# Kernel optimization log

Measured on AMD Instinct MI355X. Metric: run time of the kernel, lower is better.

The kernel has to match this reference:

```python
import jax, jax.numpy as jnp
import numpy as np

NUM_STAB = 1e-3  # numerical_stabilizer for relu kernel


def _relu_feature(x, proj):
    # x: [B, L, H, D], proj: [M, D] -> [B, L, H, M]
    ratio = 1.0 / jnp.sqrt(jnp.asarray(proj.shape[0], x.dtype))
    return jax.nn.relu(ratio * jnp.einsum('blhd,md->blhm', x, proj)) + NUM_STAB


def setup_inputs() -> dict:
    key = jax.random.key(0)
    k1, k2, k3, k4, k5 = jax.random.split(key, 5)
    B, L, H, D, M = 16, 576, 12, 64, 8  # L = length_of_side**2 = 24**2
    return {
        'query': jax.random.normal(k1, (B, L, H, D), dtype=jnp.float32),
        'key': jax.random.normal(k2, (B, L, H, D), dtype=jnp.float32),
        'value': jax.random.normal(k3, (B, L, H, D), dtype=jnp.float32),
        'projection_matrix': jax.random.normal(k4, (M, D), dtype=jnp.float32),
        # RPE mask is nonnegative per-head mixing matrix [H, L, L]
        'mask_matrix': jax.random.uniform(k5, (H, L, L), dtype=jnp.float32),
    }


def reference(query, key, value, projection_matrix, mask_matrix):
    # ReLU kernel features (projection_matrix_type='relu')
    q_prime = _relu_feature(query, projection_matrix)  # [B, L, H, M]
    k_prime = _relu_feature(key, projection_matrix)    # [B, L, H, M]
    B, L, H, M = k_prime.shape
    D = value.shape[-1]

    # D_1[b,l,h,m,d] = k'[b,l,h,m] * v[b,l,h,d], flattened over (m,d)
    D_1 = jnp.einsum('blhm,blhd->blhmd', k_prime, value).reshape(B, L, H, M * D)
    # mask-matrix causal/RPE mixing over the L dimension (per head)
    D_1_hat = jnp.einsum('hij,bjhc->bihc', mask_matrix, D_1).reshape(B, L, H, M, D)
    D_2_hat = jnp.einsum('hij,bjhm->bihm', mask_matrix, k_prime)  # [B, L, H, M]

    av_attention = jnp.einsum('blhm,blhmd->blhd', q_prime, D_1_hat)  # [B, L, H, D]
    ks_sum = jnp.sum(D_2_hat, axis=1)                                # [B, H, M]
    normalizer = jnp.einsum('blhm,bhm->blh', q_prime, ks_sum)        # [B, L, H]
    return av_attention / normalizer[..., None]
```

## Files before the change

kernel.cpp:

```cpp
#include <hip/hip_runtime.h>
#include <hip/hip_bf16.h>


#define B_ 16
#define L_ 576
#define H_ 12
#define D_ 64
#define M_ 8
#define NUM_STAB 1e-3f
#define RATIO 0.35355339059327373f

typedef __attribute__((ext_vector_type(8))) short short8;
typedef __attribute__((ext_vector_type(4))) float f32x4;

union Pack {
    uint4 u4;
    short8 s8;
    uint2 u2[2];
    unsigned u[4];
    unsigned short us[8];
};

__device__ inline unsigned short f2bf(float x) {
    union { float f; unsigned u; } a; a.f = x;
    unsigned r = (a.u + 0x7FFFu + ((a.u >> 16) & 1u)) >> 16;
    return (unsigned short)r;
}
__device__ inline unsigned pk2(float lo, float hi) {
    __hip_bfloat162 h = __float22bfloat162_rn(make_float2(lo, hi));
    union { __hip_bfloat162 b; unsigned u; } c; c.b = h;
    return c.u;
}
__device__ inline float bf2f(unsigned short u) {
    union { unsigned u; float f; } c; c.u = (unsigned)u << 16; return c.f;
}

#define WS_W_OFF  (H_ * L_)
#define WS_QP_OFF (H_ * L_ + B_ * H_ * M_)
#define QP_ELEMS  ((size_t)B_ * H_ * L_ * M_)

__global__ __launch_bounds__(256) void feat_kernel(const float* __restrict__ q,
                                                   const float* __restrict__ k,
                                                   const float* __restrict__ proj,
                                                   const float* __restrict__ mask,
                                                   unsigned short* __restrict__ qp,
                                                   unsigned short* __restrict__ kp,
                                                   float* __restrict__ cmask) {
    __shared__ float cred[4][16];
    const int lc = blockIdx.x, h = blockIdx.y, b = blockIdx.z, t = threadIdx.x;
    const int wv = t >> 6, l = t & 63, r8 = l >> 3, c8 = l & 7;
    const int row = lc * 32 + wv * 8 + r8;

    float4 pj0[8], pj1[8];
#pragma unroll
    for (int m = 0; m < 8; ++m) {
        pj0[m] = *(const float4*)(proj + m * 64 + c8 * 8);
        pj1[m] = *(const float4*)(proj + m * 64 + c8 * 8 + 4);
    }

#pragma unroll
    for (int s = 0; s < 2; ++s) {
        const float* src = s ? k : q;
        unsigned short* dst = s ? kp : qp;
        const float* xp = src + (((size_t)b * L_ + row) * H_ + h) * D_ + c8 * 8;
        float4 x0 = *(const float4*)xp;
        float4 x1 = *(const float4*)(xp + 4);
        x0.x *= RATIO; x0.y *= RATIO; x0.z *= RATIO; x0.w *= RATIO;
        x1.x *= RATIO; x1.y *= RATIO; x1.z *= RATIO; x1.w *= RATIO;
        float p[8];
#pragma unroll
        for (int m = 0; m < 8; ++m) {
            p[m] = x0.x * pj0[m].x + x0.y * pj0[m].y + x0.z * pj0[m].z + x0.w * pj0[m].w
                 + x1.x * pj1[m].x + x1.y * pj1[m].y + x1.z * pj1[m].z + x1.w * pj1[m].w;
        }
#pragma unroll
        for (int st = 1; st <= 4; st <<= 1) {
#pragma unroll
            for (int m = 0; m < 8; ++m) p[m] += __shfl_xor(p[m], st, 64);
        }
        float r = p[0];
        r = (c8 == 1) ? p[1] : r;
        r = (c8 == 2) ? p[2] : r;
        r = (c8 == 3) ? p[3] : r;
        r = (c8 == 4) ? p[4] : r;
        r = (c8 == 5) ? p[5] : r;
        r = (c8 == 6) ? p[6] : r;
        r = (c8 == 7) ? p[7] : r;
        r = fmaxf(r, 0.f) + NUM_STAB;
        dst[((size_t)(b * H_ + h) * L_ + row) * 8 + c8] = f2bf(r);
    }

    if (b < 2) {
        const int c = t & 15, rg = t >> 4;
        const int col0 = lc * 32 + b * 16;
        const float* mb = mask + (size_t)h * L_ * L_ + col0 + c;
        float a = 0.f;
#pragma unroll 4
        for (int k2 = 0; k2 < 36; ++k2) a += mb[(size_t)(rg + 16 * k2) * L_];
        a += __shfl_xor(a, 16, 64);
        a += __shfl_xor(a, 32, 64);
        if ((l >> 4) == 0) cred[wv][c] = a;
        __syncthreads();
        if (t < 16) cmask[h * L_ + col0 + t] = cred[0][t] + cred[1][t] + cred[2][t] + cred[3][t];
    }
}

__global__ __launch_bounds__(64) void wsum_kernel(const unsigned short* __restrict__ kp,
                                                  const float* __restrict__ cmask,
                                                  float* __restrict__ wbuf) {
    const int bh = blockIdx.x, lx = threadIdx.x;
    const int h = bh % H_;
    const unsigned short* kpb = kp + (size_t)bh * L_ * 8;
    const float* cm = cmask + h * L_;
    float a[8] = {0.f, 0.f, 0.f, 0.f, 0.f, 0.f, 0.f, 0.f};
    for (int j = lx; j < L_; j += 64) {
        const float c = cm[j];
        Pack pk; pk.u4 = *(const uint4*)(kpb + (size_t)j * 8);
#pragma unroll
        for (int m = 0; m < 8; ++m) a[m] += c * bf2f(pk.us[m]);
    }
#pragma unroll
    for (int st = 1; st < 64; st <<= 1) {
#pragma unroll
        for (int m = 0; m < 8; ++m) a[m] += __shfl_xor(a[m], st, 64);
    }
    float r = a[0];
    r = (lx == 1) ? a[1] : r;
    r = (lx == 2) ? a[2] : r;
    r = (lx == 3) ? a[3] : r;
    r = (lx == 4) ? a[4] : r;
    r = (lx == 5) ? a[5] : r;
    r = (lx == 6) ? a[6] : r;
    r = (lx == 7) ? a[7] : r;
    if (lx < 8) wbuf[(size_t)bh * 8 + lx] = r;
}

__global__ __launch_bounds__(256, 4) void attn_kernel(const float* __restrict__ v,
                                                      const float* __restrict__ mask,
                                                      const unsigned short* __restrict__ qp,
                                                      const unsigned short* __restrict__ kp,
                                                      const float* __restrict__ wbuf,
                                                      float* __restrict__ out) {
    __shared__ __align__(16) unsigned short Sp[2][4][16 * 64];

    const int t = threadIdx.x;
    const int n = blockIdx.x;
    const int vid = (n & 7) * 216 + (n >> 3);
    const int b = vid & 15;
    const int g = vid >> 4;
    const int it = g % 9, h = g / 9;
    const int i0 = it * 64;

    const int wv = t >> 6, l = t & 63, c15 = l & 15, kq = l >> 4;
    const int sxor = (c15 & 7) << 4;

    const float* maskbase = mask + (size_t)h * L_ * L_ + (size_t)(i0 + 16 * wv + c15) * L_ + 4 * kq;
    const unsigned short* kpb = kp + (size_t)(b * H_ + h) * L_ * 8;
    const float* vbase = v + ((size_t)b * L_ * H_ + h) * D_ + 16 * wv + c15;

    short8 Bq;
    {
        Pack pk; pk.u4 = make_uint4(0, 0, 0, 0);
        if (kq == 0)
            pk.u4 = *(const uint4*)(qp + ((size_t)(b * H_ + h) * L_ + i0 + 16 * wv + c15) * 8);
        Bq = pk.s8;
    }

    f32x4 acc0 = {0.f, 0.f, 0.f, 0.f}, acc1 = acc0, acc2 = acc0, acc3 = acc0;
    const f32x4 zz = {0.f, 0.f, 0.f, 0.f};

    uint4 a0 = make_uint4(0, 0, 0, 0), a1 = a0, a2 = a0, a3 = a0;
    float vf0[8], vf1[8];
    float4 mvb[2][4];

    if (kq == 0) {
        a0 = *(const uint4*)(kpb + (size_t)(c15) * 8);
        a1 = *(const uint4*)(kpb + (size_t)(16 + c15) * 8);
        a2 = *(const uint4*)(kpb + (size_t)(32 + c15) * 8);
        a3 = *(const uint4*)(kpb + (size_t)(48 + c15) * 8);
    }
#pragma unroll
    for (int e = 0; e < 8; ++e) vf0[e] = vbase[(size_t)(kq * 8 + e) * (H_ * D_)];
#pragma unroll
    for (int e = 0; e < 8; ++e) vf1[e] = vbase[(size_t)(32 + kq * 8 + e) * (H_ * D_)];
#pragma unroll
    for (int T = 0; T < 4; ++T) mvb[0][T] = *(const float4*)(maskbase + 16 * T);
#pragma unroll
    for (int T = 0; T < 4; ++T) mvb[1][T] = *(const float4*)(maskbase + 64 + 16 * T);

#pragma unroll
    for (int jt = 0; jt < 9; ++jt) {
        const int slab = jt & 1;
        char* SpW = (char*)Sp[slab][wv];

        f32x4 s0, s1, s2, s3;
        {
            Pack p0, p1, p2, p3;
            p0.u4 = a0; p1.u4 = a1; p2.u4 = a2; p3.u4 = a3;
            s0 = __builtin_amdgcn_mfma_f32_16x16x32_bf16(p0.s8, Bq, zz, 0, 0, 0);
            s1 = __builtin_amdgcn_mfma_f32_16x16x32_bf16(p1.s8, Bq, zz, 0, 0, 0);
            s2 = __builtin_amdgcn_mfma_f32_16x16x32_bf16(p2.s8, Bq, zz, 0, 0, 0);
            s3 = __builtin_amdgcn_mfma_f32_16x16x32_bf16(p3.s8, Bq, zz, 0, 0, 0);
        }

        {
            const float4 m0 = mvb[jt & 1][0], m1 = mvb[jt & 1][1];
            const float4 m2 = mvb[jt & 1][2], m3 = mvb[jt & 1][3];
            const int sb = c15 * 128 + 8 * kq;
            uint2 st2;
            st2.x = pk2(s0[0] * m0.x, s0[1] * m0.y);
            st2.y = pk2(s0[2] * m0.z, s0[3] * m0.w);
            *(uint2*)(SpW + ((sb + 0) ^ sxor)) = st2;
            st2.x = pk2(s1[0] * m1.x, s1[1] * m1.y);
            st2.y = pk2(s1[2] * m1.z, s1[3] * m1.w);
            *(uint2*)(SpW + ((sb + 32) ^ sxor)) = st2;
            st2.x = pk2(s2[0] * m2.x, s2[1] * m2.y);
            st2.y = pk2(s2[2] * m2.z, s2[3] * m2.w);
            *(uint2*)(SpW + ((sb + 64) ^ sxor)) = st2;
            st2.x = pk2(s3[0] * m3.x, s3[1] * m3.y);
            st2.y = pk2(s3[2] * m3.z, s3[3] * m3.w);
            *(uint2*)(SpW + ((sb + 96) ^ sxor)) = st2;
        }

        Pack bv0, bv1;
#pragma unroll
        for (int q4 = 0; q4 < 4; ++q4) bv0.u[q4] = pk2(vf0[2 * q4], vf0[2 * q4 + 1]);
#pragma unroll
        for (int q4 = 0; q4 < 4; ++q4) bv1.u[q4] = pk2(vf1[2 * q4], vf1[2 * q4 + 1]);

        asm volatile("s_waitcnt lgkmcnt(0)\n\ts_barrier" ::: "memory");

        {
            const int j1 = ((jt < 8) ? jt + 1 : 0) * 64;
            const int j2 = ((jt < 7) ? jt + 2 : 0) * 64;
            if (kq == 0) {
                a0 = *(const uint4*)(kpb + (size_t)(j1 + c15) * 8);
                a1 = *(const uint4*)(kpb + (size_t)(j1 + 16 + c15) * 8);
                a2 = *(const uint4*)(kpb + (size_t)(j1 + 32 + c15) * 8);
                a3 = *(const uint4*)(kpb + (size_t)(j1 + 48 + c15) * 8);
            }
#pragma unroll
            for (int e = 0; e < 8; ++e) vf0[e] = vbase[(size_t)(j1 + kq * 8 + e) * (H_ * D_)];
#pragma unroll
            for (int e = 0; e < 8; ++e) vf1[e] = vbase[(size_t)(j1 + 32 + kq * 8 + e) * (H_ * D_)];
#pragma unroll
            for (int T = 0; T < 4; ++T) mvb[jt & 1][T] = *(const float4*)(maskbase + j2 + 16 * T);
        }

        {
            const char* SpR = (const char*)Sp[slab][0];
            const int rb = c15 * 128;
#pragma unroll
            for (int iw = 0; iw < 4; ++iw) {
                const char* ch = SpR + iw * 2048;
                short8 As0 = *(const short8*)(ch + ((rb + 16 * kq) ^ sxor));
                short8 As1 = *(const short8*)(ch + ((rb + 64 + 16 * kq) ^ sxor));
                f32x4* ap = (iw == 0) ? &acc0 : (iw == 1) ? &acc1 : (iw == 2) ? &acc2 : &acc3;
                *ap = __builtin_amdgcn_mfma_f32_16x16x32_bf16(As0, bv0.s8, *ap, 0, 0, 0);
                *ap = __builtin_amdgcn_mfma_f32_16x16x32_bf16(As1, bv1.s8, *ap, 0, 0, 0);
            }
        }
    }

    const float* wp = wbuf + (size_t)(b * H_ + h) * 8;
    const float4 w0 = *(const float4*)wp;
    const float4 w1 = *(const float4*)(wp + 4);
    const f32x4 aa[4] = {acc0, acc1, acc2, acc3};
#pragma unroll
    for (int iw = 0; iw < 4; ++iw) {
        Pack pq;
        pq.u4 = *(const uint4*)(qp + ((size_t)(b * H_ + h) * L_ + i0 + 16 * iw + c15) * 8);
        float n2 = bf2f(pq.us[0]) * w0.x + bf2f(pq.us[1]) * w0.y +
                   bf2f(pq.us[2]) * w0.z + bf2f(pq.us[3]) * w0.w +
                   bf2f(pq.us[4]) * w1.x + bf2f(pq.us[5]) * w1.y +
                   bf2f(pq.us[6]) * w1.z + bf2f(pq.us[7]) * w1.w;
        float* ob = out + (((size_t)b * L_ + i0 + 16 * iw) * H_ + h) * D_ + 16 * wv + c15;
#pragma unroll
        for (int r = 0; r < 4; ++r) {
            float iv = 1.0f / __shfl(n2, 4 * kq + r, 64);
            ob[(size_t)(4 * kq + r) * (H_ * D_)] = aa[iw][r] * iv;
        }
    }
}

extern "C" void kernel_launch(void* const* d_in, const int* in_sizes, int n_in,
                              void* d_out, int out_size, void* d_ws, size_t ws_size,
                              hipStream_t stream) {
    const float* q    = (const float*)d_in[0];
    const float* k    = (const float*)d_in[1];
    const float* v    = (const float*)d_in[2];
    const float* proj = (const float*)d_in[3];
    const float* mask = (const float*)d_in[4];
    float* out = (float*)d_out;

    float* ws = (float*)d_ws;
    float* cmask = ws;
    float* wbuf  = ws + WS_W_OFF;
    unsigned short* qp_w = (unsigned short*)(ws + WS_QP_OFF);
    unsigned short* kp_w = qp_w + QP_ELEMS;

    feat_kernel<<<dim3(L_ / 32, H_, B_), 256, 0, stream>>>(q, k, proj, mask, qp_w, kp_w, cmask);
    wsum_kernel<<<B_ * H_, 64, 0, stream>>>(kp_w, cmask, wbuf);
    attn_kernel<<<1728, 256, 0, stream>>>(v, mask, qp_w, kp_w, wbuf, out);
}
```

Measured before the change: 188.8 us.

## Switch attention to 32x32 MFMA with register shuffles and pre-packed bf16 V

The feature kernel now also converts V to bf16 pairs, interleaved along L, into a workspace buffer. The attention kernel moves from 16x16x32 MFMAs with a double-buffered LDS staging of the masked scores to 32x32x16 MFMAs. The masked score fragment is rearranged into the A operand with cross-half-wave shuffles, which removes shared memory and the per-tile barrier. In exchange it adds an extra write and read of V in bf16 through global memory, and each wave now covers 32 rows by 32 columns.

```diff
diff --git a/kernel.cpp b/kernel.cpp
--- a/kernel.cpp
+++ b/kernel.cpp
@@ -12,11 +12,11 @@
 
 typedef __attribute__((ext_vector_type(8))) short short8;
 typedef __attribute__((ext_vector_type(4))) float f32x4;
+typedef __attribute__((ext_vector_type(16))) float f32x16;
 
 union Pack {
     uint4 u4;
     short8 s8;
-    uint2 u2[2];
     unsigned u[4];
     unsigned short us[8];
 };
@@ -38,14 +38,17 @@
 #define WS_W_OFF  (H_ * L_)
 #define WS_QP_OFF (H_ * L_ + B_ * H_ * M_)
 #define QP_ELEMS  ((size_t)B_ * H_ * L_ * M_)
+#define VT2_PER_BH (288 * 64)
 
 __global__ __launch_bounds__(256) void feat_kernel(const float* __restrict__ q,
                                                    const float* __restrict__ k,
+                                                   const float* __restrict__ v,
                                                    const float* __restrict__ proj,
                                                    const float* __restrict__ mask,
                                                    unsigned short* __restrict__ qp,
                                                    unsigned short* __restrict__ kp,
-                                                   float* __restrict__ cmask) {
+                                                   float* __restrict__ cmask,
+                                                   unsigned* __restrict__ vt2) {
     __shared__ float cred[4][16];
     const int lc = blockIdx.x, h = blockIdx.y, b = blockIdx.z, t = threadIdx.x;
     const int wv = t >> 6, l = t & 63, r8 = l >> 3, c8 = l & 7;
@@ -88,6 +91,18 @@
         r = (c8 == 7) ? p[7] : r;
         r = fmaxf(r, 0.f) + NUM_STAB;
         dst[((size_t)(b * H_ + h) * L_ + row) * 8 + c8] = f2bf(r);
+    }
+
+    {
+        const int dv = t & 63, wv2 = t >> 6;
+        unsigned* vw = vt2 + (size_t)(b * H_ + h) * VT2_PER_BH;
+#pragma unroll
+        for (int rr = 0; rr < 4; ++rr) {
+            const int j2 = lc * 16 + rr * 4 + wv2;
+            const float* vs = v + (((size_t)b * L_ + 2 * j2) * H_ + h) * D_ + dv;
+            float v0 = vs[0], v1 = vs[H_ * D_];
+            vw[(size_t)j2 * 64 + dv] = pk2(v0, v1);
+        }
     }
 
     if (b < 2) {
@@ -135,151 +150,118 @@
     if (lx < 8) wbuf[(size_t)bh * 8 + lx] = r;
 }
 
-__global__ __launch_bounds__(256, 4) void attn_kernel(const float* __restrict__ v,
-                                                      const float* __restrict__ mask,
+__global__ __launch_bounds__(256, 4) void attn_kernel(const float* __restrict__ mask,
                                                       const unsigned short* __restrict__ qp,
                                                       const unsigned short* __restrict__ kp,
+                                                      const unsigned* __restrict__ vt2,
                                                       const float* __restrict__ wbuf,
                                                       float* __restrict__ out) {
-    __shared__ __align__(16) unsigned short Sp[2][4][16 * 64];
-
     const int t = threadIdx.x;
     const int n = blockIdx.x;
     const int vid = (n & 7) * 216 + (n >> 3);
     const int b = vid & 15;
     const int g = vid >> 4;
     const int it = g % 9, h = g / 9;
-    const int i0 = it * 64;
-
-    const int wv = t >> 6, l = t & 63, c15 = l & 15, kq = l >> 4;
-    const int sxor = (c15 & 7) << 4;
-
-    const float* maskbase = mask + (size_t)h * L_ * L_ + (size_t)(i0 + 16 * wv + c15) * L_ + 4 * kq;
-    const unsigned short* kpb = kp + (size_t)(b * H_ + h) * L_ * 8;
-    const float* vbase = v + ((size_t)b * L_ * H_ + h) * D_ + 16 * wv + c15;
+
+    const int wv = t >> 6, ln = t & 63, li = ln & 31, hx = ln >> 5;
+    const bool hi = (hx != 0);
+    const int iw = wv >> 1, dw = wv & 1;
+    const int i0 = it * 64 + iw * 32;
+    const int d0 = dw * 32;
+    const int bh = b * H_ + h;
+
+    const unsigned short* kpb = kp + (size_t)bh * L_ * 8;
+    const float* mrow = mask + (size_t)h * L_ * L_ + (size_t)(i0 + li) * L_ + 4 * hx;
+    const unsigned* vp = vt2 + (size_t)bh * VT2_PER_BH + hx * (4 * 64) + d0 + li;
 
     short8 Bq;
     {
         Pack pk; pk.u4 = make_uint4(0, 0, 0, 0);
-        if (kq == 0)
-            pk.u4 = *(const uint4*)(qp + ((size_t)(b * H_ + h) * L_ + i0 + 16 * wv + c15) * 8);
+        if (!hi) pk.u4 = *(const uint4*)(qp + ((size_t)bh * L_ + i0 + li) * 8);
         Bq = pk.s8;
     }
 
-    f32x4 acc0 = {0.f, 0.f, 0.f, 0.f}, acc1 = acc0, acc2 = acc0, acc3 = acc0;
-    const f32x4 zz = {0.f, 0.f, 0.f, 0.f};
-
-    uint4 a0 = make_uint4(0, 0, 0, 0), a1 = a0, a2 = a0, a3 = a0;
-    float vf0[8], vf1[8];
-    float4 mvb[2][4];
-
-    if (kq == 0) {
-        a0 = *(const uint4*)(kpb + (size_t)(c15) * 8);
-        a1 = *(const uint4*)(kpb + (size_t)(16 + c15) * 8);
-        a2 = *(const uint4*)(kpb + (size_t)(32 + c15) * 8);
-        a3 = *(const uint4*)(kpb + (size_t)(48 + c15) * 8);
-    }
-#pragma unroll
-    for (int e = 0; e < 8; ++e) vf0[e] = vbase[(size_t)(kq * 8 + e) * (H_ * D_)];
-#pragma unroll
-    for (int e = 0; e < 8; ++e) vf1[e] = vbase[(size_t)(32 + kq * 8 + e) * (H_ * D_)];
-#pragma unroll
-    for (int T = 0; T < 4; ++T) mvb[0][T] = *(const float4*)(maskbase + 16 * T);
-#pragma unroll
-    for (int T = 0; T < 4; ++T) mvb[1][T] = *(const float4*)(maskbase + 64 + 16 * T);
-
-#pragma unroll
-    for (int jt = 0; jt < 9; ++jt) {
-        const int slab = jt & 1;
-        char* SpW = (char*)Sp[slab][wv];
-
-        f32x4 s0, s1, s2, s3;
-        {
-            Pack p0, p1, p2, p3;
-            p0.u4 = a0; p1.u4 = a1; p2.u4 = a2; p3.u4 = a3;
-            s0 = __builtin_amdgcn_mfma_f32_16x16x32_bf16(p0.s8, Bq, zz, 0, 0, 0);
-            s1 = __builtin_amdgcn_mfma_f32_16x16x32_bf16(p1.s8, Bq, zz, 0, 0, 0);
-            s2 = __builtin_amdgcn_mfma_f32_16x16x32_bf16(p2.s8, Bq, zz, 0, 0, 0);
-            s3 = __builtin_amdgcn_mfma_f32_16x16x32_bf16(p3.s8, Bq, zz, 0, 0, 0);
-        }
-
-        {
-            const float4 m0 = mvb[jt & 1][0], m1 = mvb[jt & 1][1];
-            const float4 m2 = mvb[jt & 1][2], m3 = mvb[jt & 1][3];
-            const int sb = c15 * 128 + 8 * kq;
-            uint2 st2;
-            st2.x = pk2(s0[0] * m0.x, s0[1] * m0.y);
-            st2.y = pk2(s0[2] * m0.z, s0[3] * m0.w);
-            *(uint2*)(SpW + ((sb + 0) ^ sxor)) = st2;
-            st2.x = pk2(s1[0] * m1.x, s1[1] * m1.y);
-            st2.y = pk2(s1[2] * m1.z, s1[3] * m1.w);
-            *(uint2*)(SpW + ((sb + 32) ^ sxor)) = st2;
-            st2.x = pk2(s2[0] * m2.x, s2[1] * m2.y);
-            st2.y = pk2(s2[2] * m2.z, s2[3] * m2.w);
-            *(uint2*)(SpW + ((sb + 64) ^ sxor)) = st2;
-            st2.x = pk2(s3[0] * m3.x, s3[1] * m3.y);
-            st2.y = pk2(s3[2] * m3.z, s3[3] * m3.w);
-            *(uint2*)(SpW + ((sb + 96) ^ sxor)) = st2;
-        }
-
-        Pack bv0, bv1;
-#pragma unroll
-        for (int q4 = 0; q4 < 4; ++q4) bv0.u[q4] = pk2(vf0[2 * q4], vf0[2 * q4 + 1]);
-#pragma unroll
-        for (int q4 = 0; q4 < 4; ++q4) bv1.u[q4] = pk2(vf1[2 * q4], vf1[2 * q4 + 1]);
-
-        asm volatile("s_waitcnt lgkmcnt(0)\n\ts_barrier" ::: "memory");
-
-        {
-            const int j1 = ((jt < 8) ? jt + 1 : 0) * 64;
-            const int j2 = ((jt < 7) ? jt + 2 : 0) * 64;
-            if (kq == 0) {
-                a0 = *(const uint4*)(kpb + (size_t)(j1 + c15) * 8);
-                a1 = *(const uint4*)(kpb + (size_t)(j1 + 16 + c15) * 8);
-                a2 = *(const uint4*)(kpb + (size_t)(j1 + 32 + c15) * 8);
-                a3 = *(const uint4*)(kpb + (size_t)(j1 + 48 + c15) * 8);
-            }
-#pragma unroll
-            for (int e = 0; e < 8; ++e) vf0[e] = vbase[(size_t)(j1 + kq * 8 + e) * (H_ * D_)];
-#pragma unroll
-            for (int e = 0; e < 8; ++e) vf1[e] = vbase[(size_t)(j1 + 32 + kq * 8 + e) * (H_ * D_)];
-#pragma unroll
-            for (int T = 0; T < 4; ++T) mvb[jt & 1][T] = *(const float4*)(maskbase + j2 + 16 * T);
-        }
-
-        {
-            const char* SpR = (const char*)Sp[slab][0];
-            const int rb = c15 * 128;
-#pragma unroll
-            for (int iw = 0; iw < 4; ++iw) {
-                const char* ch = SpR + iw * 2048;
-                short8 As0 = *(const short8*)(ch + ((rb + 16 * kq) ^ sxor));
-                short8 As1 = *(const short8*)(ch + ((rb + 64 + 16 * kq) ^ sxor));
-                f32x4* ap = (iw == 0) ? &acc0 : (iw == 1) ? &acc1 : (iw == 2) ? &acc2 : &acc3;
-                *ap = __builtin_amdgcn_mfma_f32_16x16x32_bf16(As0, bv0.s8, *ap, 0, 0, 0);
-                *ap = __builtin_amdgcn_mfma_f32_16x16x32_bf16(As1, bv1.s8, *ap, 0, 0, 0);
-            }
-        }
-    }
-
-    const float* wp = wbuf + (size_t)(b * H_ + h) * 8;
+    f32x16 acc = {};
+    const f32x16 zz = {};
+
+    uint4 kbuf[2];
+    float4 mbuf[2][4];
+    kbuf[0] = make_uint4(0, 0, 0, 0);
+    kbuf[1] = make_uint4(0, 0, 0, 0);
+
+    if (!hi) kbuf[0] = *(const uint4*)(kpb + (size_t)li * 8);
+    mbuf[0][0] = *(const float4*)(mrow + 0);
+    mbuf[0][1] = *(const float4*)(mrow + 8);
+    mbuf[0][2] = *(const float4*)(mrow + 16);
+    mbuf[0][3] = *(const float4*)(mrow + 24);
+
+#pragma unroll
+    for (int jt = 0; jt < 18; ++jt) {
+        const int p = jt & 1, np = p ^ 1;
+
+        const unsigned* vq = vp + (size_t)jt * 1024;
+        unsigned vb0 = vq[0],   vb1 = vq[64],  vb2 = vq[128], vb3 = vq[192];
+        unsigned vb4 = vq[512], vb5 = vq[576], vb6 = vq[640], vb7 = vq[704];
+
+        const int j1 = ((jt < 17) ? jt + 1 : 0) * 32;
+        if (!hi) kbuf[np] = *(const uint4*)(kpb + (size_t)(j1 + li) * 8);
+        mbuf[np][0] = *(const float4*)(mrow + j1 + 0);
+        mbuf[np][1] = *(const float4*)(mrow + j1 + 8);
+        mbuf[np][2] = *(const float4*)(mrow + j1 + 16);
+        mbuf[np][3] = *(const float4*)(mrow + j1 + 24);
+
+        Pack ka; ka.u4 = kbuf[p];
+        f32x16 S = __builtin_amdgcn_mfma_f32_32x32x16_bf16(ka.s8, Bq, zz, 0, 0, 0);
+
+        unsigned pk_[8];
+#pragma unroll
+        for (int r4 = 0; r4 < 4; ++r4) {
+            const float4 m4 = mbuf[p][r4];
+            pk_[2 * r4]     = pk2(S[4 * r4 + 0] * m4.x, S[4 * r4 + 1] * m4.y);
+            pk_[2 * r4 + 1] = pk2(S[4 * r4 + 2] * m4.z, S[4 * r4 + 3] * m4.w);
+        }
+
+        unsigned q0 = hi ? pk_[0] : pk_[2];
+        unsigned q1 = hi ? pk_[1] : pk_[3];
+        unsigned q2 = hi ? pk_[4] : pk_[6];
+        unsigned q3 = hi ? pk_[5] : pk_[7];
+        unsigned s0 = (unsigned)__shfl_xor((int)q0, 32, 64);
+        unsigned s1 = (unsigned)__shfl_xor((int)q1, 32, 64);
+        unsigned s2 = (unsigned)__shfl_xor((int)q2, 32, 64);
+        unsigned s3 = (unsigned)__shfl_xor((int)q3, 32, 64);
+        Pack A0, A1, V0, V1;
+        A0.u[0] = hi ? s0 : pk_[0];
+        A0.u[1] = hi ? s1 : pk_[1];
+        A0.u[2] = hi ? pk_[2] : s0;
+        A0.u[3] = hi ? pk_[3] : s1;
+        A1.u[0] = hi ? s2 : pk_[4];
+        A1.u[1] = hi ? s3 : pk_[5];
+        A1.u[2] = hi ? pk_[6] : s2;
+        A1.u[3] = hi ? pk_[7] : s3;
+        V0.u[0] = vb0; V0.u[1] = vb1; V0.u[2] = vb2; V0.u[3] = vb3;
+        V1.u[0] = vb4; V1.u[1] = vb5; V1.u[2] = vb6; V1.u[3] = vb7;
+
+        acc = __builtin_amdgcn_mfma_f32_32x32x16_bf16(A0.s8, V0.s8, acc, 0, 0, 0);
+        acc = __builtin_amdgcn_mfma_f32_32x32x16_bf16(A1.s8, V1.s8, acc, 0, 0, 0);
+    }
+
+    const float* wp = wbuf + (size_t)bh * 8;
     const float4 w0 = *(const float4*)wp;
     const float4 w1 = *(const float4*)(wp + 4);
-    const f32x4 aa[4] = {acc0, acc1, acc2, acc3};
-#pragma unroll
-    for (int iw = 0; iw < 4; ++iw) {
-        Pack pq;
-        pq.u4 = *(const uint4*)(qp + ((size_t)(b * H_ + h) * L_ + i0 + 16 * iw + c15) * 8);
-        float n2 = bf2f(pq.us[0]) * w0.x + bf2f(pq.us[1]) * w0.y +
-                   bf2f(pq.us[2]) * w0.z + bf2f(pq.us[3]) * w0.w +
-                   bf2f(pq.us[4]) * w1.x + bf2f(pq.us[5]) * w1.y +
-                   bf2f(pq.us[6]) * w1.z + bf2f(pq.us[7]) * w1.w;
-        float* ob = out + (((size_t)b * L_ + i0 + 16 * iw) * H_ + h) * D_ + 16 * wv + c15;
-#pragma unroll
-        for (int r = 0; r < 4; ++r) {
-            float iv = 1.0f / __shfl(n2, 4 * kq + r, 64);
-            ob[(size_t)(4 * kq + r) * (H_ * D_)] = aa[iw][r] * iv;
-        }
+    Pack pq;
+    pq.u4 = *(const uint4*)(qp + ((size_t)bh * L_ + i0 + li) * 8);
+    float nn = bf2f(pq.us[0]) * w0.x + bf2f(pq.us[1]) * w0.y +
+               bf2f(pq.us[2]) * w0.z + bf2f(pq.us[3]) * w0.w +
+               bf2f(pq.us[4]) * w1.x + bf2f(pq.us[5]) * w1.y +
+               bf2f(pq.us[6]) * w1.z + bf2f(pq.us[7]) * w1.w;
+    float ivn = 1.0f / nn;
+
+    float* ob = out + (((size_t)b * L_ + i0) * H_ + h) * D_ + d0 + li;
+#pragma unroll
+    for (int r = 0; r < 16; ++r) {
+        const int row = (r & 3) + 8 * (r >> 2) + 4 * hx;
+        float iv = __shfl(ivn, row, 64);
+        ob[(size_t)row * (H_ * D_)] = acc[r] * iv;
     }
 }
 
@@ -298,8 +280,9 @@
     float* wbuf  = ws + WS_W_OFF;
     unsigned short* qp_w = (unsigned short*)(ws + WS_QP_OFF);
     unsigned short* kp_w = qp_w + QP_ELEMS;
-
-    feat_kernel<<<dim3(L_ / 32, H_, B_), 256, 0, stream>>>(q, k, proj, mask, qp_w, kp_w, cmask);
+    unsigned* vt2_w = (unsigned*)(kp_w + QP_ELEMS);
+
+    feat_kernel<<<dim3(L_ / 32, H_, B_), 256, 0, stream>>>(q, k, v, proj, mask, qp_w, kp_w, cmask, vt2_w);
     wsum_kernel<<<B_ * H_, 64, 0, stream>>>(kp_w, cmask, wbuf);
-    attn_kernel<<<1728, 256, 0, stream>>>(v, mask, qp_w, kp_w, wbuf, out);
-}
+    attn_kernel<<<1728, 256, 0, stream>>>(mask, qp_w, kp_w, vt2_w, wbuf, out);
+}
```

Result: slower. 209.8 us (+11.1%).
